# Kernel tuning notes

Hardware: AMD Instinct MI355X
Metric: run time of the kernel (lower is better)

## Reference

```python
import jax, jax.numpy as jnp
import numpy as np
from jax import lax

M = 8   # num_heads
K = 4   # num_points


def conv2d(x, w, b, pad):
    # x: [B,C,H,W], w: [O,I,kh,kw]
    y = lax.conv_general_dilated(x, w, (1, 1), [(pad, pad), (pad, pad)],
                                 dimension_numbers=('NCHW', 'OIHW', 'NCHW'))
    return y + b[None, :, None, None]


def grid_sample_zeros(v, px, py):
    # Bilinear grid_sample, align_corners=True, padding_mode='zeros'.
    # v: [N,Cm,H,W]; px,py: [N,P] in pixel coordinates.
    N, Cm, H, W = v.shape
    x0 = jnp.floor(px); y0 = jnp.floor(py)
    x1 = x0 + 1.0;      y1 = y0 + 1.0
    wx = px - x0;       wy = py - y0
    vflat = v.reshape(N, Cm, H * W)

    def tap(xi, yi):
        valid = (xi >= 0) & (xi <= W - 1) & (yi >= 0) & (yi <= H - 1)
        xc = jnp.clip(xi, 0, W - 1).astype(jnp.int32)
        yc = jnp.clip(yi, 0, H - 1).astype(jnp.int32)
        idx = yc * W + xc                          # [N,P]
        g = jnp.take_along_axis(vflat, idx[:, None, :], axis=2)  # [N,Cm,P]
        return g * valid[:, None, :].astype(v.dtype)

    v00 = tap(x0, y0); v01 = tap(x1, y0)
    v10 = tap(x0, y1); v11 = tap(x1, y1)
    wx = wx[:, None, :]; wy = wy[:, None, :]
    return (v00 * (1 - wx) * (1 - wy) + v01 * wx * (1 - wy)
            + v10 * (1 - wx) * wy + v11 * wx * wy)


def setup_inputs() -> dict:
    key = jax.random.key(0)
    ks = jax.random.split(key, 16)
    B, C, H, W = 8, 256, 64, 64
    s = 0.02
    inp = {
        'f_recalib': jax.random.normal(ks[0], (B, C, H, W), jnp.float32),
        'f_orig':    jax.random.normal(ks[1], (B, C, H, W), jnp.float32),
        'offset_w': jax.random.normal(ks[2], (M * K * 2, C, 3, 3), jnp.float32) * s,
        'offset_b': jnp.zeros((M * K * 2,), jnp.float32),
        'attn_w':   jax.random.normal(ks[3], (M * K, C, 3, 3), jnp.float32) * s,
        'attn_b':   jnp.zeros((M * K,), jnp.float32),
        'value_w':  jax.random.normal(ks[4], (C, C, 1, 1), jnp.float32) * s,
        'value_b':  jnp.zeros((C,), jnp.float32),
        'proj_w':   jax.random.normal(ks[5], (C, C, 1, 1), jnp.float32) * s,
        'proj_b':   jnp.zeros((C,), jnp.float32),
        'mlp_w1':   jax.random.normal(ks[6], (2 * C, C, 1, 1), jnp.float32) * s,
        'mlp_b1':   jnp.zeros((2 * C,), jnp.float32),
        'mlp_w2':   jax.random.normal(ks[7], (C, 2 * C, 1, 1), jnp.float32) * s,
        'mlp_b2':   jnp.zeros((C,), jnp.float32),
    }
    return inp


def reference(f_recalib, f_orig, offset_w, offset_b, attn_w, attn_b,
              value_w, value_b, proj_w, proj_b,
              mlp_w1, mlp_b1, mlp_w2, mlp_b2):
    B, C, H, W = f_recalib.shape
    Cm = C // M

    offsets = conv2d(f_recalib, offset_w, offset_b, 1).reshape(B, M, K, 2, H, W)
    attn = conv2d(f_recalib, attn_w, attn_b, 1).reshape(B, M, K, H, W)
    attn = jax.nn.softmax(attn, axis=2)
    value = conv2d(f_recalib, value_w, value_b, 0)

    gy, gx = jnp.meshgrid(jnp.arange(H, dtype=jnp.float32),
                          jnp.arange(W, dtype=jnp.float32), indexing='ij')
    gx_sym = (W - 1) - gx  # horizontally mirrored x coordinate
    # pixel-space sampling locations (align_corners=True normalization is exactly
    # inverted by grid_sample's unnormalization, so work in pixel coords)
    px = gx_sym[None, None, None] + offsets[:, :, :, 0]  # [B,M,K,H,W]
    py = gy[None, None, None] + offsets[:, :, :, 1]

    v = value.reshape(B * M, Cm, H, W)
    sampled = grid_sample_zeros(v, px.reshape(B * M, -1), py.reshape(B * M, -1))
    sampled = sampled.reshape(B, M, Cm, K, H, W)

    out = (sampled * attn[:, :, None]).sum(axis=3).reshape(B, C, H, W)
    out = conv2d(out, proj_w, proj_b, 0) + f_orig
    h = jax.nn.relu(conv2d(out, mlp_w1, mlp_b1, 0))
    out = conv2d(h, mlp_w2, mlp_b2, 0) + out
    return out
```

## Files before the change

kernel.cpp:

```cpp
#include <hip/hip_runtime.h>
#include <cstddef>

#define P_ 4096
#define PW_ 66

using u16 = unsigned short;
typedef float  f32x4  __attribute__((ext_vector_type(4)));
typedef u16    u16x8  __attribute__((ext_vector_type(8)));
typedef u16    u16x4  __attribute__((ext_vector_type(4)));
typedef __bf16 bf16x8 __attribute__((ext_vector_type(8)));

#define DEVINL __device__ __forceinline__

DEVINL u16 f2bf(float f) {
    union { float f; unsigned u; } v; v.f = f;
    unsigned r = v.u + 0x7fffu + ((v.u >> 16) & 1u);
    return (u16)(r >> 16);
}
DEVINL float bf2f(u16 h) {
    union { unsigned u; float f; } v; v.u = ((unsigned)h) << 16;
    return v.f;
}

DEVINL f32x4 mfma16(u16x8 a, u16x8 b, f32x4 c) {
    return __builtin_amdgcn_mfma_f32_16x16x32_bf16(
        __builtin_bit_cast(bf16x8, a), __builtin_bit_cast(bf16x8, b), c, 0, 0, 0);
}

DEVINL void gload16(const u16* src, const u16* lds_dst) {
    __builtin_amdgcn_global_load_lds(
        (const __attribute__((address_space(1))) void*)src,
        (__attribute__((address_space(3))) void*)lds_dst, 16, 0, 0);
}

__global__ __launch_bounds__(256) void to_nhwc_pad(
    const float* __restrict__ in, u16* __restrict__ xp,
    const float* __restrict__ off_w, const float* __restrict__ attn_w,
    const float* __restrict__ val_w, const float* __restrict__ proj_w,
    const float* __restrict__ w1, const float* __restrict__ w2,
    u16* __restrict__ wbf) {
    const int bx = blockIdx.x, c0 = blockIdx.y * 64, b = blockIdx.z;
    const int t = threadIdx.x;

    if (bx >= 64) {
        const int idx = ((bx - 64) * 32 + blockIdx.y * 8 + b) * 256 + t;
        if (idx >= 614400) return;
        float v;
        if (idx < 221184) {
            int tap = idx / 24576, rem = idx - tap * 24576, oc = rem >> 8, ic = rem & 255;
            v = (oc < 64) ? off_w[(size_t)(oc * 256 + ic) * 9 + tap]
                          : attn_w[(size_t)((oc - 64) * 256 + ic) * 9 + tap];
        } else if (idx < 286720) v = val_w[idx - 221184];
        else if (idx < 352256)   v = proj_w[idx - 286720];
        else if (idx < 483328)   v = w1[idx - 352256];
        else                     v = w2[idx - 483328];
        wbf[idx] = f2bf(v);
        return;
    }

    const int y = bx;
    __shared__ u16 ts[64 * 72];
    const int cl = t >> 4, xq = t & 15;

    if (y == 0) {
        const u16x8 z = (u16x8){0, 0, 0, 0, 0, 0, 0, 0};
        for (int q = t; q < 2080; q += 256) {
            const int p = q >> 3, c8 = q & 7;
            int row, col;
            if (p < 66)       { row = 0;  col = p; }
            else if (p < 132) { row = 65; col = p - 66; }
            else { const int q2 = p - 132; row = 1 + (q2 >> 1); col = (q2 & 1) * 65; }
            *(u16x8*)&xp[((size_t)(b * PW_ + row) * PW_ + col) * 256 + c0 + c8 * 8] = z;
        }
    }

    #pragma unroll
    for (int r = 0; r < 4; ++r) {
        const int c = r * 16 + cl;
        const float4 v = *(const float4*)&in[((size_t)(b * 256 + c0 + c)) * P_ + y * 64 + xq * 4];
        ts[(xq * 4 + 0) * 72 + c] = f2bf(v.x);
        ts[(xq * 4 + 1) * 72 + c] = f2bf(v.y);
        ts[(xq * 4 + 2) * 72 + c] = f2bf(v.z);
        ts[(xq * 4 + 3) * 72 + c] = f2bf(v.w);
    }
    __syncthreads();
    const int px = t >> 2, seg = t & 3;
    u16x8 o0, o1;
    #pragma unroll
    for (int j = 0; j < 8; ++j) {
        o0[j] = ts[px * 72 + seg * 16 + j];
        o1[j] = ts[px * 72 + seg * 16 + 8 + j];
    }
    const size_t base = ((size_t)(b * PW_ + y + 1) * PW_ + 1 + px) * 256 + c0 + seg * 16;
    *(u16x8*)&xp[base]     = o0;
    *(u16x8*)&xp[base + 8] = o1;
}

__global__ __launch_bounds__(256, 2) void conv3x3_mfma(
    const u16* __restrict__ xp, const u16* __restrict__ wconv,
    const float* __restrict__ off_b, const float* __restrict__ attn_b,
    u16* __restrict__ convout) {
    const int y = blockIdx.x, b = blockIdx.y;
    const int tid = threadIdx.x, w = tid >> 6, lane = tid & 63, g = lane >> 4, i = lane & 15;
    const int wm = w & 1, wn = w >> 1;
    const int srow = lane >> 4, sc = lane & 15;
    __shared__ u16 lds[40960];

    f32x4 acc[2][3];
    #pragma unroll
    for (int mi = 0; mi < 2; ++mi)
        #pragma unroll
        for (int nj = 0; nj < 3; ++nj) acc[mi][nj] = (f32x4){0.f, 0.f, 0.f, 0.f};

    auto stage = [&](int buf, int c) {
        const int tap = c >> 1, kc = (c & 1) * 128;
        const int dy = tap / 3, dx = tap % 3;
        const u16* xrow = xp + ((size_t)(b * PW_ + y + dy) * PW_ + dx) * 256;
        const u16* wt = wconv + (size_t)(tap * 96) * 256;
        u16* bufA = &lds[buf * 8192];
        u16* bufW = &lds[16384 + buf * 12288];
        #pragma unroll
        for (int t = 0; t < 4; ++t) {
            const int j = w * 4 + t;
            const int row = j * 4 + srow;
            const int cs = sc ^ (row & 7);
            gload16(xrow + (size_t)row * 256 + kc + (cs << 3), &bufA[j * 512]);
        }
        #pragma unroll
        for (int t = 0; t < 6; ++t) {
            const int j = w * 6 + t;
            const int row = j * 4 + srow;
            const int cs = sc ^ (row & 7);
            gload16(wt + (size_t)row * 256 + kc + (cs << 3), &bufW[j * 512]);
        }
    };

    stage(0, 0);
    stage(1, 1);
    asm volatile("s_waitcnt vmcnt(10)" ::: "memory");
    __builtin_amdgcn_s_barrier();

    for (int c = 0; c < 18; ++c) {
        const u16* bufA = &lds[(c & 1) * 8192];
        const u16* bufW = &lds[16384 + (c & 1) * 12288];
        #pragma unroll
        for (int ks = 0; ks < 4; ++ks) {
            u16x8 a[2], bb[3];
            #pragma unroll
            for (int mi = 0; mi < 2; ++mi) {
                const int pr = wm * 32 + mi * 16 + i;
                a[mi] = *(const u16x8*)&bufA[pr * 128 + (((ks * 4 + g) ^ (pr & 7)) << 3)];
            }
            #pragma unroll
            for (int nj = 0; nj < 3; ++nj) {
                const int ocr = wn * 48 + nj * 16 + i;
                bb[nj] = *(const u16x8*)&bufW[ocr * 128 + (((ks * 4 + g) ^ (ocr & 7)) << 3)];
            }
            #pragma unroll
            for (int mi = 0; mi < 2; ++mi)
                #pragma unroll
                for (int nj = 0; nj < 3; ++nj)
                    acc[mi][nj] = mfma16(a[mi], bb[nj], acc[mi][nj]);
        }
        __builtin_amdgcn_sched_barrier(0);
        __builtin_amdgcn_s_barrier();
        if (c + 2 < 18) {
            stage(c & 1, c + 2);
            asm volatile("s_waitcnt vmcnt(10)" ::: "memory");
        } else {
            asm volatile("s_waitcnt vmcnt(0)" ::: "memory");
        }
        __builtin_amdgcn_s_barrier();
    }

    #pragma unroll
    for (int mi = 0; mi < 2; ++mi) {
        const int x0 = wm * 32 + mi * 16 + g * 4;
        #pragma unroll
        for (int nj = 0; nj < 3; ++nj) {
            const int oc = wn * 48 + nj * 16 + i;
            const float bv = (oc < 64) ? off_b[oc] : attn_b[oc - 64];
            #pragma unroll
            for (int r = 0; r < 4; ++r)
                convout[((size_t)(b * P_ + y * 64 + x0 + r)) * 96 + oc] =
                    f2bf(acc[mi][nj][r] + bv);
        }
    }
}

__global__ __launch_bounds__(256, 2) void gemm_dbuf(
    const u16* __restrict__ X, const u16* __restrict__ W,
    const float* __restrict__ bias, const void* __restrict__ resid,
    void* __restrict__ outA, u16* __restrict__ outB,
    const int KTOT, const int OC, const int mode, const int padded) {
    const int px0 = blockIdx.x * 128, oc0 = blockIdx.y * 128, b = blockIdx.z;
    const int tid = threadIdx.x, w = tid >> 6, lane = tid & 63, g = lane >> 4, i = lane & 15;
    const int wm = w & 1, wn = w >> 1;
    __shared__ u16 lds[32768];
    u16* xs = lds;
    u16* wsL = lds + 16384;

    const int srcC = (lane & 7) ^ ((lane >> 3) & 7);

    f32x4 acc[4][4];
    #pragma unroll
    for (int mi = 0; mi < 4; ++mi)
        #pragma unroll
        for (int nj = 0; nj < 4; ++nj) acc[mi][nj] = (f32x4){0.f, 0.f, 0.f, 0.f};

    const int NC = KTOT >> 6;

    auto stage = [&](int buf, int kc) {
        #pragma unroll
        for (int t = 0; t < 4; ++t) {
            const int j = w * 4 + t;
            const int row = j * 8 + (lane >> 3);
            const u16* sx;
            if (padded) {
                const int pxg = px0 + row;
                sx = X + ((size_t)(b * PW_ + (pxg >> 6) + 1) * PW_ + (pxg & 63) + 1) * 256
                       + kc + (srcC << 3);
            } else {
                sx = X + (size_t)(b * P_ + px0 + row) * KTOT + kc + (srcC << 3);
            }
            gload16(sx, &xs[buf * 8192 + j * 512]);
        }
        #pragma unroll
        for (int t = 0; t < 4; ++t) {
            const int j = w * 4 + t;
            const int row = j * 8 + (lane >> 3);
            gload16(W + (size_t)(oc0 + row) * KTOT + kc + (srcC << 3),
                    &wsL[buf * 8192 + j * 512]);
        }
    };

    stage(0, 0);
    stage(1, 64);
    asm volatile("s_waitcnt vmcnt(8)" ::: "memory");
    __builtin_amdgcn_s_barrier();

    for (int c = 0; c < NC; ++c) {
        const u16* xb = &xs[(c & 1) * 8192];
        const u16* wb = &wsL[(c & 1) * 8192];
        #pragma unroll
        for (int ks = 0; ks < 2; ++ks) {
            u16x8 a[4], bb[4];
            #pragma unroll
            for (int mi = 0; mi < 4; ++mi) {
                const int row = wm * 64 + mi * 16 + i;
                a[mi] = *(const u16x8*)&xb[row * 64 + (((ks * 4 + g) ^ (row & 7)) << 3)];
            }
            #pragma unroll
            for (int nj = 0; nj < 4; ++nj) {
                const int row = wn * 64 + nj * 16 + i;
                bb[nj] = *(const u16x8*)&wb[row * 64 + (((ks * 4 + g) ^ (row & 7)) << 3)];
            }
            #pragma unroll
            for (int mi = 0; mi < 4; ++mi)
                #pragma unroll
                for (int nj = 0; nj < 4; ++nj)
                    acc[mi][nj] = mfma16(a[mi], bb[nj], acc[mi][nj]);
        }
        __builtin_amdgcn_sched_barrier(0);
        __builtin_amdgcn_s_barrier();
        if (c + 2 < NC) {
            stage(c & 1, (c + 2) << 6);
            asm volatile("s_waitcnt vmcnt(8)" ::: "memory");
        } else {
            asm volatile("s_waitcnt vmcnt(0)" ::: "memory");
        }
        __builtin_amdgcn_s_barrier();
    }

    float* lf = (float*)lds;
    const int pxq = tid >> 2, segq = tid & 3;
    const int oclh = tid >> 1, shh = (tid & 1) * 32;

    #pragma unroll
    for (int h = 0; h < 2; ++h) {
        if (wm == h) {
            #pragma unroll
            for (int nj = 0; nj < 4; ++nj) {
                const int ocl = wn * 64 + nj * 16 + i;
                const float bv = bias[oc0 + ocl];
                #pragma unroll
                for (int mi = 0; mi < 4; ++mi)
                    #pragma unroll
                    for (int r = 0; r < 4; ++r)
                        lf[ocl * 66 + mi * 16 + g * 4 + r] = acc[mi][nj][r] + bv;
            }
        }
        __syncthreads();
        const int pxg0 = px0 + h * 64;

        if (mode == 4) {
            const float* rf = (const float*)resid;
            const size_t rb = ((size_t)b * 256 + oc0 + oclh) * P_ + pxg0 + shh;
            #pragma unroll
            for (int q = 0; q < 8; ++q) {
                const float4 r4 = *(const float4*)&rf[rb + q * 4];
                lf[oclh * 66 + shh + q * 4 + 0] += r4.x;
                lf[oclh * 66 + shh + q * 4 + 1] += r4.y;
                lf[oclh * 66 + shh + q * 4 + 2] += r4.z;
                lf[oclh * 66 + shh + q * 4 + 3] += r4.w;
            }
            __syncthreads();
        }

        if (mode <= 1 || mode == 4) {
            const size_t nb = ((size_t)(b * P_ + pxg0 + pxq)) * OC + oc0 + segq * 32;
            #pragma unroll
            for (int t2 = 0; t2 < 4; ++t2) {
                u16x8 o8;
                #pragma unroll
                for (int jj = 0; jj < 8; ++jj) {
                    float v = lf[(segq * 32 + t2 * 8 + jj) * 66 + pxq];
                    if (mode == 1) v = fmaxf(v, 0.f);
                    o8[jj] = f2bf(v);
                }
                *(u16x8*)&outB[nb + t2 * 8] = o8;
            }
        }
        if (mode == 4) {
            u16* on = (u16*)outA;
            const size_t cb = ((size_t)b * 256 + oc0 + oclh) * P_ + pxg0 + shh;
            #pragma unroll
            for (int t2 = 0; t2 < 4; ++t2) {
                u16x8 o8;
                #pragma unroll
                for (int jj = 0; jj < 8; ++jj)
                    o8[jj] = f2bf(lf[oclh * 66 + shh + t2 * 8 + jj]);
                *(u16x8*)&on[cb + t2 * 8] = o8;
            }
        }
        if (mode == 5) {
            const u16* rb16 = (const u16*)resid;
            float* of = (float*)outA;
            const size_t cb = ((size_t)b * 256 + oc0 + oclh) * P_ + pxg0 + shh;
            #pragma unroll
            for (int q = 0; q < 8; ++q) {
                const u16x4 r4 = *(const u16x4*)&rb16[cb + q * 4];
                float4 o;
                o.x = lf[oclh * 66 + shh + q * 4 + 0] + bf2f(r4[0]);
                o.y = lf[oclh * 66 + shh + q * 4 + 1] + bf2f(r4[1]);
                o.z = lf[oclh * 66 + shh + q * 4 + 2] + bf2f(r4[2]);
                o.w = lf[oclh * 66 + shh + q * 4 + 3] + bf2f(r4[3]);
                *(float4*)&of[cb + q * 4] = o;
            }
        }
        __syncthreads();
    }
}

__global__ __launch_bounds__(256) void sample_attend_bf(
    const u16* __restrict__ value, const u16* __restrict__ conv,
    u16* __restrict__ out1) {
    const int y = blockIdx.x, m = blockIdx.y, b = blockIdx.z;
    const int tid = threadIdx.x, x = tid >> 2, gq = tid & 3;
    const int w = tid >> 6, lane = tid & 63;
    const int wlo = max(0, y - 3), whi = min(63, y + 4);
    const int nchunks = (whi - wlo + 1) * 256;
    __shared__ u16 vlds[8 * 64 * 32];

    const u16* vbase = value + ((size_t)b * P_) * 256 + m * 32;
    for (int it = w; it * 64 < nchunks; it += 4) {
        const int cid = it * 64 + lane;
        const int r = cid >> 8, px = (cid >> 2) & 63, cc = cid & 3;
        gload16(vbase + ((size_t)((wlo + r) * 64 + px)) * 256 + cc * 8,
                &vlds[it * 512]);
    }

    const size_t prow = (size_t)(b * P_ + y * 64 + x);
    const u16x8 ov = *(const u16x8*)&conv[prow * 96 + m * 8];
    const u16x4 av = *(const u16x4*)&conv[prow * 96 + 64 + m * 4];
    float a[4];
    #pragma unroll
    for (int k = 0; k < 4; ++k) a[k] = bf2f(av[k]);
    const float mx = fmaxf(fmaxf(a[0], a[1]), fmaxf(a[2], a[3]));
    float s = 0.f;
    #pragma unroll
    for (int k = 0; k < 4; ++k) { a[k] = __expf(a[k] - mx); s += a[k]; }
    const float inv = 1.f / s;

    __syncthreads();

    float acc[8];
    #pragma unroll
    for (int j = 0; j < 8; ++j) acc[j] = 0.f;

    #pragma unroll
    for (int k = 0; k < 4; ++k) {
        const float offx = bf2f(ov[2 * k]), offy = bf2f(ov[2 * k + 1]);
        const float px = (float)(63 - x) + offx;
        const float py = (float)y + offy;
        const float x0f = floorf(px), y0f = floorf(py);
        const int xi0 = (int)x0f, yi0 = (int)y0f;
        const float wx = px - x0f, wy = py - y0f;
        const int xi1 = xi0 + 1, yi1 = yi0 + 1;
        const bool vx0 = (xi0 >= 0) & (xi0 <= 63), vx1 = (xi1 >= 0) & (xi1 <= 63);
        const bool vy0 = (yi0 >= 0) & (yi0 <= 63), vy1 = (yi1 >= 0) & (yi1 <= 63);
        const int cx0 = min(max(xi0, 0), 63), cx1 = min(max(xi1, 0), 63);
        const int cy0 = min(max(yi0, 0), 63), cy1 = min(max(yi1, 0), 63);
        const float ak = a[k] * inv;
        const float c00 = ak * (1.f - wx) * (1.f - wy) * ((vx0 & vy0) ? 1.f : 0.f);
        const float c01 = ak * wx * (1.f - wy) * ((vx1 & vy0) ? 1.f : 0.f);
        const float c10 = ak * (1.f - wx) * wy * ((vx0 & vy1) ? 1.f : 0.f);
        const float c11 = ak * wx * wy * ((vx1 & vy1) ? 1.f : 0.f);
        u16x8 v00, v01, v10, v11;
        const bool inWin = (cy0 >= wlo) & (cy1 <= whi);
        if (inWin) {
            const int r0 = (cy0 - wlo) * 64, r1 = (cy1 - wlo) * 64;
            v00 = *(const u16x8*)&vlds[(r0 + cx0) * 32 + gq * 8];
            v01 = *(const u16x8*)&vlds[(r0 + cx1) * 32 + gq * 8];
            v10 = *(const u16x8*)&vlds[(r1 + cx0) * 32 + gq * 8];
            v11 = *(const u16x8*)&vlds[(r1 + cx1) * 32 + gq * 8];
        } else {
            const u16* vb = vbase + gq * 8;
            v00 = *(const u16x8*)&vb[(size_t)(cy0 * 64 + cx0) * 256];
            v01 = *(const u16x8*)&vb[(size_t)(cy0 * 64 + cx1) * 256];
            v10 = *(const u16x8*)&vb[(size_t)(cy1 * 64 + cx0) * 256];
            v11 = *(const u16x8*)&vb[(size_t)(cy1 * 64 + cx1) * 256];
        }
        #pragma unroll
        for (int j = 0; j < 8; ++j)
            acc[j] += c00 * bf2f(v00[j]) + c01 * bf2f(v01[j])
                    + c10 * bf2f(v10[j]) + c11 * bf2f(v11[j]);
    }
    u16x8 o;
    #pragma unroll
    for (int j = 0; j < 8; ++j) o[j] = f2bf(acc[j]);
    *(u16x8*)&out1[prow * 256 + m * 32 + gq * 8] = o;
}

extern "C" void kernel_launch(void* const* d_in, const int* in_sizes, int n_in,
                              void* d_out, int out_size, void* d_ws, size_t ws_size,
                              hipStream_t stream) {
    const float* f_recalib = (const float*)d_in[0];
    const float* f_orig    = (const float*)d_in[1];
    const float* offset_w  = (const float*)d_in[2];
    const float* offset_b  = (const float*)d_in[3];
    const float* attn_w    = (const float*)d_in[4];
    const float* attn_b    = (const float*)d_in[5];
    const float* value_w   = (const float*)d_in[6];
    const float* value_b   = (const float*)d_in[7];
    const float* proj_w    = (const float*)d_in[8];
    const float* proj_b    = (const float*)d_in[9];
    const float* mlp_w1    = (const float*)d_in[10];
    const float* mlp_b1    = (const float*)d_in[11];
    const float* mlp_w2    = (const float*)d_in[12];
    const float* mlp_b2    = (const float*)d_in[13];
    float* out = (float*)d_out;

    u16* wsb       = (u16*)d_ws;
    u16* x_pad     = wsb;
    u16* convout   = wsb + 8921088;
    u16* value_bf  = wsb + 12066816;
    u16* out1_bf   = wsb + 20455424;
    u16* wbf       = wsb + 28844032;
    u16* out2_nchw = wsb + 29458432;
    u16* out2_bf   = x_pad;
    u16* h_bf      = wsb + 8921088;

    u16* wconv = wbf;
    u16* wval  = wbf + 221184;
    u16* wproj = wbf + 286720;
    u16* wmlp1 = wbf + 352256;
    u16* wmlp2 = wbf + 483328;

    to_nhwc_pad<<<dim3(139, 4, 8), 256, 0, stream>>>(
        f_recalib, x_pad, offset_w, attn_w, value_w, proj_w, mlp_w1, mlp_w2, wbf);
    conv3x3_mfma<<<dim3(64, 8), 256, 0, stream>>>(x_pad, wconv, offset_b, attn_b, convout);
    gemm_dbuf<<<dim3(32, 2, 8), 256, 0, stream>>>(x_pad, wval, value_b, nullptr,
                                                  nullptr, value_bf, 256, 256, 0, 1);
    sample_attend_bf<<<dim3(64, 8, 8), 256, 0, stream>>>(value_bf, convout, out1_bf);
    gemm_dbuf<<<dim3(32, 2, 8), 256, 0, stream>>>(out1_bf, wproj, proj_b, f_orig,
                                                  out2_nchw, out2_bf, 256, 256, 4, 0);
    gemm_dbuf<<<dim3(32, 4, 8), 256, 0, stream>>>(out2_bf, wmlp1, mlp_b1, nullptr,
                                                  nullptr, h_bf, 256, 512, 1, 0);
    gemm_dbuf<<<dim3(32, 2, 8), 256, 0, stream>>>(h_bf, wmlp2, mlp_b2, out2_nchw,
                                                  out, nullptr, 512, 256, 5, 0);
}
```

Baseline: 143.7 us.

## Fuse value 1x1 projection into 3x3 conv kernel and drop NCHW residual copy

Measured after the change: 144.4 us. Within noise of the previous version (+0.5%).

```diff
diff --git a/kernel.cpp b/kernel.cpp
--- a/kernel.cpp
+++ b/kernel.cpp
@@ -98,8 +98,10 @@
 
 __global__ __launch_bounds__(256, 2) void conv3x3_mfma(
     const u16* __restrict__ xp, const u16* __restrict__ wconv,
+    const u16* __restrict__ wval,
     const float* __restrict__ off_b, const float* __restrict__ attn_b,
-    u16* __restrict__ convout) {
+    const float* __restrict__ val_b,
+    u16* __restrict__ convout, u16* __restrict__ value_bf) {
     const int y = blockIdx.x, b = blockIdx.y;
     const int tid = threadIdx.x, w = tid >> 6, lane = tid & 63, g = lane >> 4, i = lane & 15;
     const int wm = w & 1, wn = w >> 1;
@@ -111,6 +113,11 @@
     for (int mi = 0; mi < 2; ++mi)
         #pragma unroll
         for (int nj = 0; nj < 3; ++nj) acc[mi][nj] = (f32x4){0.f, 0.f, 0.f, 0.f};
+    f32x4 accv[2][8];
+    #pragma unroll
+    for (int mi = 0; mi < 2; ++mi)
+        #pragma unroll
+        for (int nj = 0; nj < 8; ++nj) accv[mi][nj] = (f32x4){0.f, 0.f, 0.f, 0.f};
 
     auto stage = [&](int buf, int c) {
         const int tap = c >> 1, kc = (c & 1) * 128;
@@ -143,6 +150,8 @@
     for (int c = 0; c < 18; ++c) {
         const u16* bufA = &lds[(c & 1) * 8192];
         const u16* bufW = &lds[16384 + (c & 1) * 12288];
+        const int kcv = (c & 1) * 128;
+        const bool doval = (c == 8) | (c == 9);
         #pragma unroll
         for (int ks = 0; ks < 4; ++ks) {
             u16x8 a[2], bb[3];
@@ -161,6 +170,16 @@
                 #pragma unroll
                 for (int nj = 0; nj < 3; ++nj)
                     acc[mi][nj] = mfma16(a[mi], bb[nj], acc[mi][nj]);
+            if (doval) {
+                #pragma unroll
+                for (int nj = 0; nj < 8; ++nj) {
+                    const int oc = wn * 128 + nj * 16 + i;
+                    const u16x8 bv = *(const u16x8*)&wval[(size_t)oc * 256 + kcv
+                                                          + ks * 32 + g * 8];
+                    accv[0][nj] = mfma16(a[0], bv, accv[0][nj]);
+                    accv[1][nj] = mfma16(a[1], bv, accv[1][nj]);
+                }
+            }
         }
         __builtin_amdgcn_sched_barrier(0);
         __builtin_amdgcn_s_barrier();
@@ -185,6 +204,15 @@
                 convout[((size_t)(b * P_ + y * 64 + x0 + r)) * 96 + oc] =
                     f2bf(acc[mi][nj][r] + bv);
         }
+        #pragma unroll
+        for (int nj = 0; nj < 8; ++nj) {
+            const int oc = wn * 128 + nj * 16 + i;
+            const float bv = val_b[oc];
+            #pragma unroll
+            for (int r = 0; r < 4; ++r)
+                value_bf[((size_t)(b * P_ + y * 64 + x0 + r)) * 256 + oc] =
+                    f2bf(accv[mi][nj][r] + bv);
+        }
     }
 }
 
@@ -192,7 +220,7 @@
     const u16* __restrict__ X, const u16* __restrict__ W,
     const float* __restrict__ bias, const void* __restrict__ resid,
     void* __restrict__ outA, u16* __restrict__ outB,
-    const int KTOT, const int OC, const int mode, const int padded) {
+    const int KTOT, const int OC, const int mode) {
     const int px0 = blockIdx.x * 128, oc0 = blockIdx.y * 128, b = blockIdx.z;
     const int tid = threadIdx.x, w = tid >> 6, lane = tid & 63, g = lane >> 4, i = lane & 15;
     const int wm = w & 1, wn = w >> 1;
@@ -215,15 +243,8 @@
         for (int t = 0; t < 4; ++t) {
             const int j = w * 4 + t;
             const int row = j * 8 + (lane >> 3);
-            const u16* sx;
-            if (padded) {
-                const int pxg = px0 + row;
-                sx = X + ((size_t)(b * PW_ + (pxg >> 6) + 1) * PW_ + (pxg & 63) + 1) * 256
-                       + kc + (srcC << 3);
-            } else {
-                sx = X + (size_t)(b * P_ + px0 + row) * KTOT + kc + (srcC << 3);
-            }
-            gload16(sx, &xs[buf * 8192 + j * 512]);
+            gload16(X + (size_t)(b * P_ + px0 + row) * KTOT + kc + (srcC << 3),
+                    &xs[buf * 8192 + j * 512]);
         }
         #pragma unroll
         for (int t = 0; t < 4; ++t) {
@@ -306,6 +327,18 @@
             }
             __syncthreads();
         }
+        if (mode == 6) {
+            const u16* rn = (const u16*)resid;
+            const size_t nb = ((size_t)(b * P_ + pxg0 + pxq)) * 256 + oc0 + segq * 32;
+            #pragma unroll
+            for (int t2 = 0; t2 < 4; ++t2) {
+                const u16x8 r8 = *(const u16x8*)&rn[nb + t2 * 8];
+                #pragma unroll
+                for (int jj = 0; jj < 8; ++jj)
+                    lf[(segq * 32 + t2 * 8 + jj) * 66 + pxq] += bf2f(r8[jj]);
+            }
+            __syncthreads();
+        }
 
         if (mode <= 1 || mode == 4) {
             const size_t nb = ((size_t)(b * P_ + pxg0 + pxq)) * OC + oc0 + segq * 32;
@@ -321,30 +354,16 @@
                 *(u16x8*)&outB[nb + t2 * 8] = o8;
             }
         }
-        if (mode == 4) {
-            u16* on = (u16*)outA;
-            const size_t cb = ((size_t)b * 256 + oc0 + oclh) * P_ + pxg0 + shh;
-            #pragma unroll
-            for (int t2 = 0; t2 < 4; ++t2) {
-                u16x8 o8;
-                #pragma unroll
-                for (int jj = 0; jj < 8; ++jj)
-                    o8[jj] = f2bf(lf[oclh * 66 + shh + t2 * 8 + jj]);
-                *(u16x8*)&on[cb + t2 * 8] = o8;
-            }
-        }
-        if (mode == 5) {
-            const u16* rb16 = (const u16*)resid;
+        if (mode == 6) {
             float* of = (float*)outA;
             const size_t cb = ((size_t)b * 256 + oc0 + oclh) * P_ + pxg0 + shh;
             #pragma unroll
             for (int q = 0; q < 8; ++q) {
-                const u16x4 r4 = *(const u16x4*)&rb16[cb + q * 4];
                 float4 o;
-                o.x = lf[oclh * 66 + shh + q * 4 + 0] + bf2f(r4[0]);
-                o.y = lf[oclh * 66 + shh + q * 4 + 1] + bf2f(r4[1]);
-                o.z = lf[oclh * 66 + shh + q * 4 + 2] + bf2f(r4[2]);
-                o.w = lf[oclh * 66 + shh + q * 4 + 3] + bf2f(r4[3]);
+                o.x = lf[oclh * 66 + shh + q * 4 + 0];
+                o.y = lf[oclh * 66 + shh + q * 4 + 1];
+                o.z = lf[oclh * 66 + shh + q * 4 + 2];
+                o.w = lf[oclh * 66 + shh + q * 4 + 3];
                 *(float4*)&of[cb + q * 4] = o;
             }
         }
@@ -457,7 +476,6 @@
     u16* value_bf  = wsb + 12066816;
     u16* out1_bf   = wsb + 20455424;
     u16* wbf       = wsb + 28844032;
-    u16* out2_nchw = wsb + 29458432;
     u16* out2_bf   = x_pad;
     u16* h_bf      = wsb + 8921088;
 
@@ -469,14 +487,13 @@
 
     to_nhwc_pad<<<dim3(139, 4, 8), 256, 0, stream>>>(
         f_recalib, x_pad, offset_w, attn_w, value_w, proj_w, mlp_w1, mlp_w2, wbf);
-    conv3x3_mfma<<<dim3(64, 8), 256, 0, stream>>>(x_pad, wconv, offset_b, attn_b, convout);
-    gemm_dbuf<<<dim3(32, 2, 8), 256, 0, stream>>>(x_pad, wval, value_b, nullptr,
-                                                  nullptr, value_bf, 256, 256, 0, 1);
+    conv3x3_mfma<<<dim3(64, 8), 256, 0, stream>>>(
+        x_pad, wconv, wval, offset_b, attn_b, value_b, convout, value_bf);
     sample_attend_bf<<<dim3(64, 8, 8), 256, 0, stream>>>(value_bf, convout, out1_bf);
     gemm_dbuf<<<dim3(32, 2, 8), 256, 0, stream>>>(out1_bf, wproj, proj_b, f_orig,
-                                                  out2_nchw, out2_bf, 256, 256, 4, 0);
+                                                  nullptr, out2_bf, 256, 256, 4);
     gemm_dbuf<<<dim3(32, 4, 8), 256, 0, stream>>>(out2_bf, wmlp1, mlp_b1, nullptr,
-                                                  nullptr, h_bf, 256, 512, 1, 0);
-    gemm_dbuf<<<dim3(32, 2, 8), 256, 0, stream>>>(h_bf, wmlp2, mlp_b2, out2_nchw,
-                                                  out, nullptr, 512, 256, 5, 0);
-}
+                                                  nullptr, h_bf, 256, 512, 1);
+    gemm_dbuf<<<dim3(32, 2, 8), 256, 0, stream>>>(h_bf, wmlp2, mlp_b2, out2_bf,
+                                                  out, nullptr, 512, 256, 6);
+}
```
